# Optimization experiments

Hardware: AMD Instinct MI355X
Metric: run time of the kernel (lower is better)

## Reference

```python
import jax, jax.numpy as jnp
import numpy as np

S, B, QD, VD, E = 2048, 32, 1024, 1024, 1024


def setup_inputs() -> dict:
    key = jax.random.key(0)
    ks = jax.random.split(key, 8)
    query = jax.random.normal(ks[0], (B, QD), dtype=jnp.float32)
    value = jax.random.normal(ks[1], (S, B, VD), dtype=jnp.float32)
    key_padding_mask = jnp.zeros((S, B), dtype=bool)
    # learned params, init as in reset_parameters()
    Wq = jax.random.uniform(ks[2], (E, QD), minval=-0.1, maxval=0.1, dtype=jnp.float32)
    Wv = jax.random.uniform(ks[3], (E, VD), minval=-0.1, maxval=0.1, dtype=jnp.float32)
    v = jax.random.uniform(ks[4], (E,), minval=-0.1, maxval=0.1, dtype=jnp.float32)
    b = jnp.zeros((E,), dtype=jnp.float32)
    g = jnp.full((1,), float(np.sqrt(1.0 / E)), dtype=jnp.float32)
    return {"query": query, "value": value, "Wq": Wq, "Wv": Wv, "v": v, "b": b, "g": g,
            "key_padding_mask": key_padding_mask}


def reference(query, value, Wq, Wv, v, b, g, key_padding_mask):
    # projected_query: (B, E) -> broadcast over seq dim
    pq = query @ Wq.T
    # key: (S, B, E)
    key = jnp.einsum('sbd,ed->sbe', value, Wv)
    normed_v = g * v / jnp.linalg.norm(v)  # (E,)
    # additive (Bahdanau) scores: (S, B)
    attn_scores = jnp.einsum('e,sbe->sb', normed_v, jnp.tanh(pq[None, :, :] + key + b))
    attn_scores = jnp.where(key_padding_mask, -jnp.inf, attn_scores)
    attn_scores = jax.nn.softmax(attn_scores, axis=0)  # softmax over seq dim
    context = jnp.einsum('sb,sbd->bd', attn_scores, value)  # (B, VD)
    return (context, attn_scores, attn_scores)
```

## Files before the change

kernel.cpp:

```cpp
#include <hip/hip_runtime.h>
#include <hip/hip_bf16.h>
#include <stdint.h>

#define SEQ 2048
#define BAT 32
#define EDIM 1024
#define MROWS (SEQ*BAT)

typedef __bf16 bf16x8 __attribute__((ext_vector_type(8)));
typedef float f32x4 __attribute__((ext_vector_type(4)));
typedef unsigned short u16x8 __attribute__((ext_vector_type(8)));

typedef __attribute__((address_space(3))) unsigned int lds_uint;
typedef const __attribute__((address_space(1))) unsigned int glb_uint;

__device__ __forceinline__ void async16(void* lds, const void* g) {
  __builtin_amdgcn_global_load_lds((glb_uint*)g, (lds_uint*)lds, 16, 0, 0);
}

__device__ __forceinline__ unsigned short f2bf(float f) {
  unsigned u = __builtin_bit_cast(unsigned, f);
  u = (u + 0x7FFFu + ((u >> 16) & 1u)) >> 16;
  return (unsigned short)u;
}
__device__ __forceinline__ float bf2f(unsigned short h) {
  return __builtin_bit_cast(float, (unsigned)h << 16);
}

__device__ __forceinline__ float fast_tanh(float x) {
  float xc = fminf(fmaxf(x, -9.f), 9.f);
  float e = __expf(2.f * xc);
  return (e - 1.f) * __builtin_amdgcn_rcpf(e + 1.f);
}

__global__ void k_nv(const float* __restrict__ v, const float* __restrict__ g,
                     float* __restrict__ nv) {
  __shared__ float red[256];
  int t = threadIdx.x;
  float s = 0.f;
  for (int i = t; i < EDIM; i += 256) { float x = v[i]; s += x * x; }
  red[t] = s; __syncthreads();
  for (int o = 128; o > 0; o >>= 1) {
    if (t < o) red[t] += red[t + o];
    __syncthreads();
  }
  float scale = g[0] / sqrtf(red[0]);
  for (int i = t; i < EDIM; i += 256) nv[i] = v[i] * scale;
}

__global__ void k_pqb(const float* __restrict__ query, const float* __restrict__ Wq,
                      const float* __restrict__ bias, float* __restrict__ pqb) {
  __shared__ float wq[1024];
  int e = blockIdx.x;
  int t = threadIdx.x;
  reinterpret_cast<float4*>(wq)[t] =
      reinterpret_cast<const float4*>(Wq + (size_t)e * EDIM)[t];
  __syncthreads();
  int w = t >> 6, lane = t & 63;
  float be = bias[e];
  for (int bb = 0; bb < 8; ++bb) {
    int b_ = w * 8 + bb;
    const float4* q4 = reinterpret_cast<const float4*>(query + (size_t)b_ * EDIM) + lane * 4;
    const float4* w4 = reinterpret_cast<const float4*>(wq) + lane * 4;
    float s = 0.f;
#pragma unroll
    for (int j = 0; j < 4; ++j) {
      float4 a = q4[j], c = w4[j];
      s += a.x * c.x + a.y * c.y + a.z * c.z + a.w * c.w;
    }
#pragma unroll
    for (int m = 32; m > 0; m >>= 1) s += __shfl_xor(s, m);
    if (lane == 0) pqb[(size_t)b_ * EDIM + e] = s + be;
  }
}

__global__ void k_cvt(const float* __restrict__ in, unsigned short* __restrict__ out,
                      long long n8) {
  long long i = (long long)blockIdx.x * blockDim.x + threadIdx.x;
  long long stride = (long long)gridDim.x * blockDim.x;
  for (; i < n8; i += stride) {
    const float4* p = reinterpret_cast<const float4*>(in + i * 8);
    float4 a = p[0], b = p[1];
    u16x8 r;
    r[0] = f2bf(a.x); r[1] = f2bf(a.y); r[2] = f2bf(a.z); r[3] = f2bf(a.w);
    r[4] = f2bf(b.x); r[5] = f2bf(b.y); r[6] = f2bf(b.z); r[7] = f2bf(b.w);
    *reinterpret_cast<u16x8*>(out + i * 8) = r;
  }
}

__global__ __launch_bounds__(256, 4) void k_gemm(
    const unsigned short* __restrict__ A,
    const unsigned short* __restrict__ Bm,
    const float* __restrict__ pqb,
    const float* __restrict__ nv,
    float* __restrict__ part)
{
  __shared__ unsigned short As[128 * 64];
  __shared__ unsigned short Bs[128 * 64];
  __shared__ float partLds[2][128];

  const int tid = threadIdx.x;
  const int lane = tid & 63;
  const int wave = tid >> 6;
  const int wm = wave >> 1, wn = wave & 1;

  const int bid = blockIdx.x;
  const int x = bid & 7;
  const int j = bid >> 3;
  const int mi_blk = x * 64 + (j >> 3);
  const int ni_blk = j & 7;
  const size_t m0 = (size_t)mi_blk * 128;
  const int n0 = ni_blk * 128;

  f32x4 acc[4][4];
#pragma unroll
  for (int i = 0; i < 4; ++i)
#pragma unroll
    for (int jj = 0; jj < 4; ++jj) acc[i][jj] = f32x4{0.f, 0.f, 0.f, 0.f};

  const int srow = tid >> 3;
  const int scol = (tid & 7) * 8;

  for (int kt = 0; kt < 16; ++kt) {
    const int k0 = kt * 64;
#pragma unroll
    for (int i = 0; i < 4; ++i) {
      async16(&As[i * 2048 + tid * 8],
              A + (m0 + (size_t)(i * 32 + srow)) * 1024 + k0 + scol);
      async16(&Bs[i * 2048 + tid * 8],
              Bm + ((size_t)(n0 + i * 32 + srow)) * 1024 + k0 + scol);
    }
    __syncthreads();
#pragma unroll
    for (int kk = 0; kk < 2; ++kk) {
      bf16x8 af[4], bfr[4];
#pragma unroll
      for (int mi = 0; mi < 4; ++mi) {
        int row = wm * 64 + mi * 16 + (lane & 15);
        af[mi] = *reinterpret_cast<const bf16x8*>(&As[row * 64 + kk * 32 + ((lane >> 4) * 8)]);
      }
#pragma unroll
      for (int nidx = 0; nidx < 4; ++nidx) {
        int row = wn * 64 + nidx * 16 + (lane & 15);
        bfr[nidx] = *reinterpret_cast<const bf16x8*>(&Bs[row * 64 + kk * 32 + ((lane >> 4) * 8)]);
      }
#pragma unroll
      for (int mi = 0; mi < 4; ++mi)
#pragma unroll
        for (int nidx = 0; nidx < 4; ++nidx)
          acc[mi][nidx] = __builtin_amdgcn_mfma_f32_16x16x32_bf16(af[mi], bfr[nidx], acc[mi][nidx], 0, 0, 0);
    }
    __syncthreads();
  }

  const int cgrp = lane >> 4;
  const int ccol = lane & 15;
  float nve[4];
#pragma unroll
  for (int nidx = 0; nidx < 4; ++nidx) nve[nidx] = nv[n0 + wn * 64 + nidx * 16 + ccol];

#pragma unroll
  for (int mi = 0; mi < 4; ++mi) {
#pragma unroll
    for (int r = 0; r < 4; ++r) {
      int rloc = wm * 64 + mi * 16 + cgrp * 4 + r;
      int b_ = rloc & 31;
      const float* pq = pqb + (size_t)b_ * EDIM + n0 + wn * 64 + ccol;
      float s = 0.f;
#pragma unroll
      for (int nidx = 0; nidx < 4; ++nidx) {
        float xin = acc[mi][nidx][r] + pq[nidx * 16];
        s += nve[nidx] * fast_tanh(xin);
      }
      s += __shfl_xor(s, 1);
      s += __shfl_xor(s, 2);
      s += __shfl_xor(s, 4);
      s += __shfl_xor(s, 8);
      if (ccol == 0) partLds[wn][rloc] = s;
    }
  }
  __syncthreads();
  if (tid < 128)
    part[(size_t)ni_blk * MROWS + m0 + tid] = partLds[0][tid] + partLds[1][tid];
}

__global__ void k_softmax(const float* __restrict__ part,
                          const unsigned char* __restrict__ mask,
                          float* __restrict__ scores,
                          float* __restrict__ out_attn)
{
  int b_ = blockIdx.x;
  int t = threadIdx.x;
  __shared__ float red[256];
  float sc[8];
  float mx = -1e30f;
#pragma unroll
  for (int i = 0; i < 8; ++i) {
    int s_ = t + i * 256;
    size_t r = (size_t)s_ * BAT + b_;
    float v = 0.f;
#pragma unroll
    for (int c = 0; c < 8; ++c) v += part[(size_t)c * MROWS + r];
    if (mask[r]) v = -1e30f;
    sc[i] = v;
    mx = fmaxf(mx, v);
  }
  red[t] = mx; __syncthreads();
  for (int o = 128; o > 0; o >>= 1) {
    if (t < o) red[t] = fmaxf(red[t], red[t + o]);
    __syncthreads();
  }
  mx = red[0];
  __syncthreads();
  float sum = 0.f;
#pragma unroll
  for (int i = 0; i < 8; ++i) { sc[i] = expf(sc[i] - mx); sum += sc[i]; }
  red[t] = sum; __syncthreads();
  for (int o = 128; o > 0; o >>= 1) {
    if (t < o) red[t] += red[t + o];
    __syncthreads();
  }
  float inv = 1.f / red[0];
#pragma unroll
  for (int i = 0; i < 8; ++i) {
    int s_ = t + i * 256;
    size_t r = (size_t)s_ * BAT + b_;
    float w = sc[i] * inv;
    scores[r] = w;
    out_attn[r] = w;
    out_attn[MROWS + r] = w;
  }
}

__global__ void k_ctx(const unsigned short* __restrict__ Vb,
                      const float* __restrict__ scores,
                      float* __restrict__ pctx)
{
  int b_ = blockIdx.x;
  int sch = blockIdx.y;
  int t = threadIdx.x;
  int d8 = t & 127;
  int sr = t >> 7;
  float acc[8];
#pragma unroll
  for (int j = 0; j < 8; ++j) acc[j] = 0.f;
  int s0 = sch * 256;
  for (int i = 0; i < 128; ++i) {
    int s_ = s0 + i * 2 + sr;
    size_t r = (size_t)s_ * BAT + b_;
    float w = scores[r];
    u16x8 v = *reinterpret_cast<const u16x8*>(Vb + r * 1024 + d8 * 8);
#pragma unroll
    for (int j = 0; j < 8; ++j) acc[j] += w * bf2f(v[j]);
  }
  float* dst = pctx + ((size_t)(sch * 2 + sr) * BAT + b_) * 1024 + d8 * 8;
#pragma unroll
  for (int j = 0; j < 8; ++j) dst[j] = acc[j];
}

__global__ void k_ctx_reduce(const float* __restrict__ pctx, float* __restrict__ out) {
  int i = blockIdx.x * 256 + threadIdx.x;
  float s = 0.f;
#pragma unroll
  for (int c = 0; c < 16; ++c) s += pctx[(size_t)c * 32768 + i];
  out[i] = s;
}

extern "C" void kernel_launch(void* const* d_in, const int* in_sizes, int n_in,
                              void* d_out, int out_size, void* d_ws, size_t ws_size,
                              hipStream_t stream) {
  const float* query = (const float*)d_in[0];
  const float* value = (const float*)d_in[1];
  const float* Wq    = (const float*)d_in[2];
  const float* Wv    = (const float*)d_in[3];
  const float* v     = (const float*)d_in[4];
  const float* bias  = (const float*)d_in[5];
  const float* g     = (const float*)d_in[6];
  const unsigned char* mask = (const unsigned char*)d_in[7];
  float* out = (float*)d_out;

  char* ws = (char*)d_ws;
  unsigned short* Vb  = (unsigned short*)ws;
  unsigned short* Wvb = (unsigned short*)(ws + (size_t)134217728);
  float* pqb    = (float*)(ws + (size_t)134217728 + 2097152);
  float* nv     = pqb + 32 * 1024;
  float* part   = nv + 1024;
  float* scores = part + 8 * MROWS;
  float* pctx   = scores + MROWS;

  k_nv<<<1, 256, 0, stream>>>(v, g, nv);
  k_pqb<<<1024, 256, 0, stream>>>(query, Wq, bias, pqb);
  k_cvt<<<2048, 256, 0, stream>>>(value, Vb, (long long)(65536LL * 1024 / 8));
  k_cvt<<<512, 256, 0, stream>>>(Wv, Wvb, (long long)(1024LL * 1024 / 8));
  k_gemm<<<4096, 256, 0, stream>>>(Vb, Wvb, pqb, nv, part);
  k_softmax<<<32, 256, 0, stream>>>(part, mask, scores, out + 32768);
  dim3 gf(32, 8);
  k_ctx<<<gf, 256, 0, stream>>>(Vb, scores, pctx);
  k_ctx_reduce<<<128, 256, 0, stream>>>(pctx, out);
}
```

Before: 312.9 us.

## Enlarge GEMM tile to 256x256 with double-buffered swizzled LDS pipeline

The fused projection+tanh GEMM now uses 512-thread blocks computing 256x256 tiles instead of 128x128, which halves the number of N-partial score buffers. LDS is double-buffered so the next K-slice is loaded asynchronously while MFMAs run on the current one, and the row layout is XOR-swizzled to avoid bank conflicts. MFMA sections are raised in priority with s_setprio. The aim is more operand reuse and overlap of global loads with compute, at the cost of higher register pressure, only one block per CU (launch bounds 512,1) and 128KB+ of LDS.

```diff
diff --git a/kernel.cpp b/kernel.cpp
--- a/kernel.cpp
+++ b/kernel.cpp
@@ -88,67 +88,110 @@
   }
 }
 
-__global__ __launch_bounds__(256, 4) void k_gemm(
+__global__ __launch_bounds__(512, 1) void k_gemm(
     const unsigned short* __restrict__ A,
     const unsigned short* __restrict__ Bm,
     const float* __restrict__ pqb,
     const float* __restrict__ nv,
     float* __restrict__ part)
 {
-  __shared__ unsigned short As[128 * 64];
-  __shared__ unsigned short Bs[128 * 64];
-  __shared__ float partLds[2][128];
+  __shared__ char smem[2 * 65536 + 4 * 256 * 4];
 
   const int tid = threadIdx.x;
   const int lane = tid & 63;
-  const int wave = tid >> 6;
-  const int wm = wave >> 1, wn = wave & 1;
+  const int wid = tid >> 6;
+  const int wm = wid >> 2;
+  const int wn = wid & 3;
 
   const int bid = blockIdx.x;
   const int x = bid & 7;
   const int j = bid >> 3;
-  const int mi_blk = x * 64 + (j >> 3);
-  const int ni_blk = j & 7;
-  const size_t m0 = (size_t)mi_blk * 128;
-  const int n0 = ni_blk * 128;
-
-  f32x4 acc[4][4];
-#pragma unroll
-  for (int i = 0; i < 4; ++i)
+  const int mi_blk = x * 32 + (j >> 2);
+  const int ni_blk = j & 3;
+  const size_t m0 = (size_t)mi_blk * 256;
+  const int n0 = ni_blk * 256;
+
+  float* partLds = (float*)(smem + 131072);
+
+  f32x4 acc[8][4];
+#pragma unroll
+  for (int i = 0; i < 8; ++i)
 #pragma unroll
     for (int jj = 0; jj < 4; ++jj) acc[i][jj] = f32x4{0.f, 0.f, 0.f, 0.f};
 
-  const int srow = tid >> 3;
-  const int scol = (tid & 7) * 8;
-
-  for (int kt = 0; kt < 16; ++kt) {
-    const int k0 = kt * 64;
+  const int cs0 = (lane >> 4) ^ (lane & 7);
+  const int cs1 = cs0 ^ 4;
+  const int rA = lane & 15;
+
+  auto stageA = [&](int slot, int k0) {
 #pragma unroll
     for (int i = 0; i < 4; ++i) {
-      async16(&As[i * 2048 + tid * 8],
-              A + (m0 + (size_t)(i * 32 + srow)) * 1024 + k0 + scol);
-      async16(&Bs[i * 2048 + tid * 8],
-              Bm + ((size_t)(n0 + i * 32 + srow)) * 1024 + k0 + scol);
-    }
-    __syncthreads();
+      int chunk = i * 512 + tid;
+      int row = chunk >> 3;
+      int csrc = (chunk & 7) ^ (row & 7);
+      async16(smem + slot * 65536 + chunk * 16,
+              A + (m0 + (size_t)row) * 1024 + k0 + csrc * 8);
+    }
+  };
+  auto stageB = [&](int slot, int k0) {
+#pragma unroll
+    for (int i = 0; i < 4; ++i) {
+      int chunk = i * 512 + tid;
+      int row = chunk >> 3;
+      int csrc = (chunk & 7) ^ (row & 7);
+      async16(smem + slot * 65536 + 32768 + chunk * 16,
+              Bm + (size_t)(n0 + row) * 1024 + k0 + csrc * 8);
+    }
+  };
+
+  stageA(0, 0);
+  stageB(0, 0);
+  __syncthreads();
+
+#pragma unroll 1
+  for (int t = 0; t < 16; ++t) {
+    char* cb = smem + (t & 1) * 65536;
+    const int nslot = (t + 1) & 1;
+    const int nk0 = (t + 1) * 64;
+    const bool pf = (t + 1) < 16;
+
+    if (pf) stageA(nslot, nk0);
+
 #pragma unroll
     for (int kk = 0; kk < 2; ++kk) {
-      bf16x8 af[4], bfr[4];
-#pragma unroll
-      for (int mi = 0; mi < 4; ++mi) {
-        int row = wm * 64 + mi * 16 + (lane & 15);
-        af[mi] = *reinterpret_cast<const bf16x8*>(&As[row * 64 + kk * 32 + ((lane >> 4) * 8)]);
-      }
-#pragma unroll
-      for (int nidx = 0; nidx < 4; ++nidx) {
-        int row = wn * 64 + nidx * 16 + (lane & 15);
-        bfr[nidx] = *reinterpret_cast<const bf16x8*>(&Bs[row * 64 + kk * 32 + ((lane >> 4) * 8)]);
-      }
-#pragma unroll
-      for (int mi = 0; mi < 4; ++mi)
-#pragma unroll
-        for (int nidx = 0; nidx < 4; ++nidx)
-          acc[mi][nidx] = __builtin_amdgcn_mfma_f32_16x16x32_bf16(af[mi], bfr[nidx], acc[mi][nidx], 0, 0, 0);
+      const int cs = kk ? cs1 : cs0;
+      bf16x8 af[8], bf[4];
+#pragma unroll
+      for (int mi = 0; mi < 8; ++mi)
+        af[mi] = *reinterpret_cast<const bf16x8*>(
+            cb + (wm * 128 + mi * 16 + rA) * 128 + cs * 16);
+#pragma unroll
+      for (int nj = 0; nj < 2; ++nj)
+        bf[nj] = *reinterpret_cast<const bf16x8*>(
+            cb + 32768 + (wn * 64 + nj * 16 + rA) * 128 + cs * 16);
+
+      __builtin_amdgcn_s_setprio(1);
+#pragma unroll
+      for (int mi = 0; mi < 8; ++mi)
+#pragma unroll
+        for (int nj = 0; nj < 2; ++nj)
+          acc[mi][nj] = __builtin_amdgcn_mfma_f32_16x16x32_bf16(af[mi], bf[nj], acc[mi][nj], 0, 0, 0);
+      __builtin_amdgcn_s_setprio(0);
+
+      if (kk == 0 && pf) stageB(nslot, nk0);
+
+#pragma unroll
+      for (int nj = 2; nj < 4; ++nj)
+        bf[nj] = *reinterpret_cast<const bf16x8*>(
+            cb + 32768 + (wn * 64 + nj * 16 + rA) * 128 + cs * 16);
+
+      __builtin_amdgcn_s_setprio(1);
+#pragma unroll
+      for (int mi = 0; mi < 8; ++mi)
+#pragma unroll
+        for (int nj = 2; nj < 4; ++nj)
+          acc[mi][nj] = __builtin_amdgcn_mfma_f32_16x16x32_bf16(af[mi], bf[nj], acc[mi][nj], 0, 0, 0);
+      __builtin_amdgcn_s_setprio(0);
     }
     __syncthreads();
   }
@@ -157,31 +200,30 @@
   const int ccol = lane & 15;
   float nve[4];
 #pragma unroll
-  for (int nidx = 0; nidx < 4; ++nidx) nve[nidx] = nv[n0 + wn * 64 + nidx * 16 + ccol];
-
-#pragma unroll
-  for (int mi = 0; mi < 4; ++mi) {
+  for (int nj = 0; nj < 4; ++nj) nve[nj] = nv[n0 + wn * 64 + nj * 16 + ccol];
+
+#pragma unroll
+  for (int mi = 0; mi < 8; ++mi) {
 #pragma unroll
     for (int r = 0; r < 4; ++r) {
-      int rloc = wm * 64 + mi * 16 + cgrp * 4 + r;
+      int rloc = wm * 128 + mi * 16 + cgrp * 4 + r;
       int b_ = rloc & 31;
       const float* pq = pqb + (size_t)b_ * EDIM + n0 + wn * 64 + ccol;
       float s = 0.f;
 #pragma unroll
-      for (int nidx = 0; nidx < 4; ++nidx) {
-        float xin = acc[mi][nidx][r] + pq[nidx * 16];
-        s += nve[nidx] * fast_tanh(xin);
-      }
+      for (int nj = 0; nj < 4; ++nj)
+        s += nve[nj] * fast_tanh(acc[mi][nj][r] + pq[nj * 16]);
       s += __shfl_xor(s, 1);
       s += __shfl_xor(s, 2);
       s += __shfl_xor(s, 4);
       s += __shfl_xor(s, 8);
-      if (ccol == 0) partLds[wn][rloc] = s;
+      if (ccol == 0) partLds[wn * 256 + rloc] = s;
     }
   }
   __syncthreads();
-  if (tid < 128)
-    part[(size_t)ni_blk * MROWS + m0 + tid] = partLds[0][tid] + partLds[1][tid];
+  if (tid < 256)
+    part[(size_t)ni_blk * MROWS + m0 + tid] =
+        partLds[tid] + partLds[256 + tid] + partLds[512 + tid] + partLds[768 + tid];
 }
 
 __global__ void k_softmax(const float* __restrict__ part,
@@ -200,7 +242,7 @@
     size_t r = (size_t)s_ * BAT + b_;
     float v = 0.f;
 #pragma unroll
-    for (int c = 0; c < 8; ++c) v += part[(size_t)c * MROWS + r];
+    for (int c = 0; c < 4; ++c) v += part[(size_t)c * MROWS + r];
     if (mask[r]) v = -1e30f;
     sc[i] = v;
     mx = fmaxf(mx, v);
@@ -285,14 +327,14 @@
   float* pqb    = (float*)(ws + (size_t)134217728 + 2097152);
   float* nv     = pqb + 32 * 1024;
   float* part   = nv + 1024;
-  float* scores = part + 8 * MROWS;
+  float* scores = part + 4 * MROWS;
   float* pctx   = scores + MROWS;
 
   k_nv<<<1, 256, 0, stream>>>(v, g, nv);
   k_pqb<<<1024, 256, 0, stream>>>(query, Wq, bias, pqb);
   k_cvt<<<2048, 256, 0, stream>>>(value, Vb, (long long)(65536LL * 1024 / 8));
   k_cvt<<<512, 256, 0, stream>>>(Wv, Wvb, (long long)(1024LL * 1024 / 8));
-  k_gemm<<<4096, 256, 0, stream>>>(Vb, Wvb, pqb, nv, part);
+  k_gemm<<<1024, 512, 0, stream>>>(Vb, Wvb, pqb, nv, part);
   k_softmax<<<32, 256, 0, stream>>>(part, mask, scores, out + 32768);
   dim3 gf(32, 8);
   k_ctx<<<gf, 256, 0, stream>>>(Vb, scores, pctx);
```

New measurement: 273.7 us. 12.5% less time.
